# Kernel tuning notes

Measured on AMD Instinct MI355X. Metric: run time of the kernel, lower is better.

The kernel has to match this reference:

```python
import jax, jax.numpy as jnp
import numpy as np

D, B, N, DIM, H, DH, MLP = 6, 4, 1024, 768, 12, 64, 3072
SCALE = DH ** -0.5
EPS = 1e-5


def setup_inputs() -> dict:
    key = jax.random.key(0)
    ks = jax.random.split(key, 5)
    s = 0.02
    return {
        "x": jax.random.normal(ks[0], (B, N, DIM), jnp.float32),
        "ln1_g": jnp.ones((D, DIM), jnp.float32),
        "ln1_b": jnp.zeros((D, DIM), jnp.float32),
        "wqkv": jax.random.normal(ks[1], (D, DIM, 3 * H * DH), jnp.float32) * s,
        "wo": jax.random.normal(ks[2], (D, H * DH, DIM), jnp.float32) * s,
        "bo": jnp.zeros((D, DIM), jnp.float32),
        "ln2_g": jnp.ones((D, DIM), jnp.float32),
        "ln2_b": jnp.zeros((D, DIM), jnp.float32),
        "w1": jax.random.normal(ks[3], (D, DIM, MLP), jnp.float32) * s,
        "b1": jnp.zeros((D, MLP), jnp.float32),
        "w2": jax.random.normal(ks[4], (D, MLP, DIM), jnp.float32) * s,
        "b2": jnp.zeros((D, DIM), jnp.float32),
    }


def _ln(h, g, b):
    m = h.mean(-1, keepdims=True)
    v = h.var(-1, keepdims=True)  # biased, matches torch LayerNorm
    return (h - m) / jnp.sqrt(v + EPS) * g + b


def _heads(t):
    # [b, n, h*d] -> [b, h, n, d]
    return t.reshape(B, N, H, DH).transpose(0, 2, 1, 3)


def reference(x, ln1_g, ln1_b, wqkv, wo, bo, ln2_g, ln2_b, w1, b1, w2, b2):
    def step(carry, p):
        xc, _, _ = carry
        g1, be1, Wqkv, Wo, Bo, g2, be2, W1, B1, W2, B2 = p
        h = _ln(xc, g1, be1)
        q, k, v = jnp.split(h @ Wqkv, 3, axis=-1)
        q, k, v = _heads(q), _heads(k), _heads(v)
        attn = jax.nn.softmax(jnp.einsum('bhid,bhjd->bhij', q, k) * SCALE, axis=-1)
        out = jnp.einsum('bhij,bhjd->bhid', attn, v)
        out = out.transpose(0, 2, 1, 3).reshape(B, N, H * DH)
        xc = xc + out @ Wo + Bo
        h2 = _ln(xc, g2, be2)
        xc = xc + jax.nn.gelu(h2 @ W1 + B1, approximate=False) @ W2 + B2
        return (xc, k, v), None

    kv0 = jnp.zeros((B, H, N, DH), x.dtype)
    (xf, k, v), _ = jax.lax.scan(
        step, (x, kv0, kv0),
        (ln1_g, ln1_b, wqkv, wo, bo, ln2_g, ln2_b, w1, b1, w2, b2))
    return xf, k, v
```

## Files before the change

kernel.cpp:

```cpp
#include <hip/hip_runtime.h>
#include <hip/hip_bf16.h>
#include <math.h>

typedef __bf16 bf16;
typedef __bf16 bf16x8 __attribute__((ext_vector_type(8)));
typedef float f32x4 __attribute__((ext_vector_type(4)));

enum { EPI_QKV = 0, EPI_GELU = 1 };

__device__ __forceinline__ void gload16(const void* g, void* s) {
  __builtin_amdgcn_global_load_lds((__attribute__((address_space(1))) void*)g,
                                   (__attribute__((address_space(3))) void*)s, 16, 0, 0);
}

#define MFMA16(a, b, c) __builtin_amdgcn_mfma_f32_16x16x32_bf16((a), (b), (c), 0, 0, 0)

__device__ __forceinline__ void xcd_swizzle(int& bx, int& by) {
  const int gx = gridDim.x, nwg = gx * gridDim.y;
  int bid = blockIdx.y * gx + blockIdx.x;
  if ((nwg & 7) == 0) bid = (bid & 7) * (nwg >> 3) + (bid >> 3);
  bx = bid % gx;
  by = bid / gx;
}

__global__ __launch_bounds__(256) void cast_x(const float* __restrict__ x,
                                              float* __restrict__ xq) {
  const int i = (blockIdx.x * 256 + threadIdx.x) * 4;
  float4 v = *(const float4*)(x + i);
  v.x = (float)(bf16)v.x; v.y = (float)(bf16)v.y;
  v.z = (float)(bf16)v.z; v.w = (float)(bf16)v.w;
  *(float4*)(xq + i) = v;
}

__global__ __launch_bounds__(256) void wconv_all(
    const float* __restrict__ wqkv, const float* __restrict__ wo,
    const float* __restrict__ w1, const float* __restrict__ w2,
    bf16* __restrict__ qkvT, bf16* __restrict__ woT,
    bf16* __restrict__ w1T, bf16* __restrict__ w2T, int lfix) {
  __shared__ float tile[64][65];
  const int bid = blockIdx.x, t = threadIdx.x;
  int l, r;
  if (lfix < 0) { l = bid / 1728; r = bid % 1728; } else { l = lfix; r = bid; }
  const int lo = (lfix < 0) ? l : 0;
  const float* W; bf16* Wt; int K, N, tt;
  if (r < 432)       { W = wqkv + (size_t)l * 768 * 2304; Wt = qkvT + (size_t)lo * 2304 * 768; K = 768;  N = 2304; tt = r; }
  else if (r < 576)  { W = wo   + (size_t)l * 768 * 768;  Wt = woT  + (size_t)lo * 768 * 768;  K = 768;  N = 768;  tt = r - 432; }
  else if (r < 1152) { W = w1   + (size_t)l * 768 * 3072; Wt = w1T  + (size_t)lo * 3072 * 768; K = 768;  N = 3072; tt = r - 576; }
  else               { W = w2   + (size_t)l * 3072 * 768; Wt = w2T  + (size_t)lo * 768 * 3072; K = 3072; N = 768;  tt = r - 1152; }
  const int ntx = N >> 6;
  const int n0 = (tt % ntx) * 64, k0 = (tt / ntx) * 64;
  const int cx = (t & 15) * 4, ry = t >> 4;
#pragma unroll
  for (int pp = 0; pp < 4; ++pp) {
    const int row = ry + pp * 16;
    const float4 v = *(const float4*)(W + (size_t)(k0 + row) * N + n0 + cx);
    tile[row][cx] = v.x; tile[row][cx + 1] = v.y;
    tile[row][cx + 2] = v.z; tile[row][cx + 3] = v.w;
  }
  __syncthreads();
#pragma unroll
  for (int it = 0; it < 2; ++it) {
    const int c = it * 256 + t;
    const int n = c >> 3, kc = (c & 7) * 8;
    bf16x8 v;
#pragma unroll
    for (int j = 0; j < 8; ++j) v[j] = (bf16)tile[kc + j][n];
    *(bf16x8*)(Wt + (size_t)(n0 + n) * K + k0 + kc) = v;
  }
}

__global__ __launch_bounds__(256) void ln_kernel(const float* __restrict__ x,
                                                 const float* __restrict__ g,
                                                 const float* __restrict__ b,
                                                 bf16* __restrict__ out) {
  const int row = blockIdx.x, t = threadIdx.x;
  const float* xr = x + (size_t)row * 768;
  float v0 = xr[t], v1 = xr[t + 256], v2 = xr[t + 512];
  float s = v0 + v1 + v2, sq = v0 * v0 + v1 * v1 + v2 * v2;
#pragma unroll
  for (int m = 32; m; m >>= 1) { s += __shfl_xor(s, m); sq += __shfl_xor(sq, m); }
  __shared__ float rs[4], rq[4];
  const int w = t >> 6;
  if ((t & 63) == 0) { rs[w] = s; rq[w] = sq; }
  __syncthreads();
  s = rs[0] + rs[1] + rs[2] + rs[3];
  sq = rq[0] + rq[1] + rq[2] + rq[3];
  const float mean = s * (1.f / 768.f);
  const float var = sq * (1.f / 768.f) - mean * mean;
  const float rstd = rsqrtf(var + 1e-5f);
  bf16* orow = out + (size_t)row * 768;
  orow[t]       = (bf16)((v0 - mean) * rstd * g[t]       + b[t]);
  orow[t + 256] = (bf16)((v1 - mean) * rstd * g[t + 256] + b[t + 256]);
  orow[t + 512] = (bf16)((v2 - mean) * rstd * g[t + 512] + b[t + 512]);
}

template <int EPI>
__global__ __launch_bounds__(256) void gemm_s(
    const bf16* __restrict__ A, const bf16* __restrict__ Bt,
    const float* __restrict__ bias, bf16* __restrict__ Cb,
    bf16* __restrict__ qo, bf16* __restrict__ ko_, bf16* __restrict__ vo,
    float* __restrict__ kf, float* __restrict__ vf, int wf,
    int M, int Nc, int K) {
  __shared__ __align__(16) char lds[2][2][8192];
  const int t = threadIdx.x, lane = t & 63, w = t >> 6;
  const int wr = w >> 1, wc = w & 1;
  int bx, by;
  xcd_swizzle(bx, by);
  const size_t m0 = (size_t)by * 128, n0 = (size_t)bx * 128;

  const char* ab[2]; const char* bb[2];
#pragma unroll
  for (int r = 0; r < 2; ++r) {
    int c = r * 256 + t;
    ab[r] = (const char*)(A + (m0 + (c >> 2)) * (size_t)K) + (c & 3) * 16;
    bb[r] = (const char*)(Bt + (n0 + (c >> 2)) * (size_t)K) + (c & 3) * 16;
  }

  f32x4 acc[4][4] = {};

  auto stage = [&](int buf, int tt) {
#pragma unroll
    for (int r = 0; r < 2; ++r) {
      gload16(ab[r] + (size_t)tt * 64, &lds[buf][0][r * 4096 + w * 1024]);
      gload16(bb[r] + (size_t)tt * 64, &lds[buf][1][r * 4096 + w * 1024]);
    }
  };
  auto compute = [&](int buf) {
    const char* As = lds[buf][0];
    const char* Bs = lds[buf][1];
    const int ko = (lane >> 4) * 16;
    bf16x8 af[4], fb[4];
#pragma unroll
    for (int i = 0; i < 4; ++i) {
      af[i] = *(const bf16x8*)(As + (wr * 64 + i * 16 + (lane & 15)) * 64 + ko);
      fb[i] = *(const bf16x8*)(Bs + (wc * 64 + i * 16 + (lane & 15)) * 64 + ko);
    }
#pragma unroll
    for (int mi = 0; mi < 4; ++mi)
#pragma unroll
      for (int ni = 0; ni < 4; ++ni)
        acc[mi][ni] = MFMA16(af[mi], fb[ni], acc[mi][ni]);
  };

  const int NT = K >> 5;
  stage(0, 0);
  __syncthreads();
  int cur = 0;
  for (int tt = 1; tt < NT; ++tt) {
    stage(cur ^ 1, tt);
    compute(cur);
    __syncthreads();
    cur ^= 1;
  }
  compute(cur);

#pragma unroll
  for (int mi = 0; mi < 4; ++mi) {
#pragma unroll
    for (int i = 0; i < 4; ++i) {
      size_t row = m0 + wr * 64 + mi * 16 + ((lane >> 4) << 2) + i;
#pragma unroll
      for (int ni = 0; ni < 4; ++ni) {
        size_t col = n0 + wc * 64 + ni * 16 + (lane & 15);
        float v = acc[mi][ni][i];
        if (EPI == EPI_GELU) {
          v += bias[col];
          v = 0.5f * v * (1.f + erff(v * 0.70710678118f));
          Cb[row * (size_t)Nc + col] = (bf16)v;
        } else {
          int b = (int)(row >> 10), n = (int)(row & 1023);
          int which = (int)col >= 1536 ? 2 : ((int)col >= 768 ? 1 : 0);
          int hd = (int)col - which * 768;
          int hh = hd >> 6, d = hd & 63;
          size_t dst = ((size_t)(b * 12 + hh) * 1024 + n) * 64 + d;
          if (which == 0) {
            qo[dst] = (bf16)(v * 0.125f);
          } else if (which == 1) {
            ko_[dst] = (bf16)v;
            if (wf) kf[dst] = v;
          } else {
            vo[dst] = (bf16)v;
            if (wf) vf[dst] = v;
          }
        }
      }
    }
  }
}

__global__ __launch_bounds__(256) void gemm64_s(
    const bf16* __restrict__ A, const bf16* __restrict__ Bt,
    const float* __restrict__ bias, const float* __restrict__ res,
    float* __restrict__ Cf, int M, int Nc, int K) {
  __shared__ __align__(16) char lds[2][12288];
  const int t = threadIdx.x, lane = t & 63, w = t >> 6;
  const int wr = w >> 1, wc = w & 1;
  const int l15 = lane & 15, l4 = lane >> 4;
  int bx, by;
  xcd_swizzle(bx, by);
  const size_t m0 = (size_t)by * 64, n0 = (size_t)bx * 128;

  const char* ab = (const char*)(A + (m0 + (t >> 2)) * (size_t)K) + (t & 3) * 16;
  const char* b0 = (const char*)(Bt + (n0 + (t >> 2)) * (size_t)K) + (t & 3) * 16;
  const char* b1 = (const char*)(Bt + (n0 + 64 + (t >> 2)) * (size_t)K) + (t & 3) * 16;

  f32x4 acc[2][4] = {};

  auto stage = [&](int buf, int tt) {
    gload16(ab + (size_t)tt * 64, &lds[buf][t * 16]);
    gload16(b0 + (size_t)tt * 64, &lds[buf][4096 + t * 16]);
    gload16(b1 + (size_t)tt * 64, &lds[buf][8192 + t * 16]);
  };
  auto compute = [&](int buf) {
    const char* L = lds[buf];
    const int ko = l4 * 16;
    bf16x8 fa[2], fb[4];
#pragma unroll
    for (int mi = 0; mi < 2; ++mi)
      fa[mi] = *(const bf16x8*)(L + (wr * 32 + mi * 16 + l15) * 64 + ko);
#pragma unroll
    for (int ni = 0; ni < 4; ++ni)
      fb[ni] = *(const bf16x8*)(L + 4096 + (wc * 64 + ni * 16 + l15) * 64 + ko);
#pragma unroll
    for (int mi = 0; mi < 2; ++mi)
#pragma unroll
      for (int ni = 0; ni < 4; ++ni)
        acc[mi][ni] = MFMA16(fa[mi], fb[ni], acc[mi][ni]);
  };

  const int NT = K >> 5;
  stage(0, 0);
  __syncthreads();
  int cur = 0;
  for (int tt = 1; tt < NT; ++tt) {
    stage(cur ^ 1, tt);
    compute(cur);
    __syncthreads();
    cur ^= 1;
  }
  compute(cur);

#pragma unroll
  for (int mi = 0; mi < 2; ++mi) {
#pragma unroll
    for (int i = 0; i < 4; ++i) {
      size_t row = m0 + wr * 32 + mi * 16 + l4 * 4 + i;
#pragma unroll
      for (int ni = 0; ni < 4; ++ni) {
        size_t col = n0 + wc * 64 + ni * 16 + l15;
        float v = acc[mi][ni][i] + bias[col] + res[row * (size_t)Nc + col];
        Cf[row * (size_t)Nc + col] = v;
      }
    }
  }
}

__global__ __launch_bounds__(256) void vtrans(const bf16* __restrict__ v,
                                              bf16* __restrict__ vT) {
  __shared__ bf16 tile[32][33];
  const int tx = threadIdx.x, ty = threadIdx.y;
  const int bh = blockIdx.x, n0 = blockIdx.y * 32, d0 = blockIdx.z * 32;
  const bf16* vb = v + (size_t)bh * 1024 * 64;
  bf16* vTb = vT + (size_t)bh * 64 * 1024;
#pragma unroll
  for (int r = 0; r < 4; ++r)
    tile[ty + r * 8][tx] = vb[(size_t)(n0 + ty + r * 8) * 64 + d0 + tx];
  __syncthreads();
#pragma unroll
  for (int r = 0; r < 4; ++r)
    vTb[(size_t)(d0 + ty + r * 8) * 1024 + n0 + tx] = tile[tx][ty + r * 8];
}

__global__ __launch_bounds__(64) void attn_main(const bf16* __restrict__ q,
                                                const bf16* __restrict__ k,
                                                const bf16* __restrict__ vT,
                                                float* __restrict__ pO,
                                                float* __restrict__ pM,
                                                float* __restrict__ pL) {
  __shared__ __align__(16) char Ks[16384];
  __shared__ __align__(16) char Vs[16384];
  char* Ps = Ks;
  const int bh = blockIdx.x, qb = blockIdx.y, half = blockIdx.z;
  const int lane = threadIdx.x & 63;
  const int l15 = lane & 15, l4 = lane >> 4;

  const char* kp = (const char*)(k + (size_t)bh * 1024 * 64);
  const char* vp = (const char*)(vT + (size_t)bh * 64 * 1024);

  const char* kb0 = kp + (lane >> 3) * 128 + (((lane & 7) ^ ((lane >> 3) & 7)) * 16)
                  + (size_t)half * 4 * 16384;
  const int vr0 = lane >> 4;
  const char* vb0 = vp + (size_t)vr0 * 2048 + (((lane & 15) ^ vr0) * 16) + half * 4 * 256;
  const char* vb1 = vp + (size_t)(vr0 + 4) * 2048 + (((lane & 15) ^ (vr0 + 4)) * 16)
                  + half * 4 * 256;

  bf16x8 aq[2][2];
  {
    const bf16* qbase = q + ((size_t)bh * 1024 + qb * 32) * 64;
#pragma unroll
    for (int mi = 0; mi < 2; ++mi)
#pragma unroll
      for (int ks = 0; ks < 2; ++ks)
        aq[mi][ks] = *(const bf16x8*)(qbase + (mi * 16 + l15) * 64 + ks * 32 + l4 * 8);
  }

  bf16x8 vones;
#pragma unroll
  for (int j = 0; j < 8; ++j) vones[j] = (bf16)1.0f;

  f32x4 oacc[2][4] = {};
  f32x4 lacc[2] = {};
  float mrun[2][4];
#pragma unroll
  for (int mi = 0; mi < 2; ++mi)
#pragma unroll
    for (int i = 0; i < 4; ++i) mrun[mi][i] = -1e30f;

#pragma unroll
  for (int jb = 0; jb < 4; ++jb) {
    const char* ksrc = kb0 + (size_t)jb * 16384;
#pragma unroll
    for (int r = 0; r < 16; ++r)
      gload16(ksrc + r * 1024, &Ks[r * 1024]);
    const char* vsrc0 = vb0 + jb * 256;
    const char* vsrc1 = vb1 + jb * 256;
#pragma unroll
    for (int r = 0; r < 8; ++r) {
      gload16(vsrc0 + (size_t)r * 16384, &Vs[r * 2048]);
      gload16(vsrc1 + (size_t)r * 16384, &Vs[r * 2048 + 1024]);
    }
    asm volatile("s_waitcnt vmcnt(16)" ::: "memory");
    __builtin_amdgcn_sched_barrier(0);

    f32x4 sacc[2][8] = {};
#pragma unroll
    for (int ks = 0; ks < 2; ++ks) {
#pragma unroll
      for (int ni = 0; ni < 8; ++ni) {
        const int rr = ni * 16 + l15;
        const bf16x8 bk = *(const bf16x8*)(Ks + rr * 128 + (((ks * 4 + l4) ^ (rr & 7)) * 16));
        sacc[0][ni] = MFMA16(aq[0][ks], bk, sacc[0][ni]);
        sacc[1][ni] = MFMA16(aq[1][ks], bk, sacc[1][ni]);
      }
    }

#pragma unroll
    for (int mi = 0; mi < 2; ++mi) {
#pragma unroll
      for (int i = 0; i < 4; ++i) {
        float mx = sacc[mi][0][i];
#pragma unroll
        for (int ni = 1; ni < 8; ++ni) mx = fmaxf(mx, sacc[mi][ni][i]);
#pragma unroll
        for (int sh = 8; sh; sh >>= 1) mx = fmaxf(mx, __shfl_xor(mx, sh));
        float mnew = fmaxf(mrun[mi][i], mx);
        float alpha = __expf(mrun[mi][i] - mnew);
        mrun[mi][i] = mnew;
#pragma unroll
        for (int ni = 0; ni < 8; ++ni)
          sacc[mi][ni][i] = __expf(sacc[mi][ni][i] - mnew);
#pragma unroll
        for (int ni = 0; ni < 4; ++ni) oacc[mi][ni][i] *= alpha;
        lacc[mi][i] *= alpha;
      }
    }

#pragma unroll
    for (int mi = 0; mi < 2; ++mi)
#pragma unroll
      for (int i = 0; i < 4; ++i) {
        int rowl = mi * 16 + l4 * 4 + i;
        char* prp = Ps + rowl * 256;
        int sw = rowl & 7;
#pragma unroll
        for (int ni = 0; ni < 8; ++ni) {
          int col = ni * 16 + l15;
          *(bf16*)(prp + (((col >> 3) ^ sw) * 16) + (col & 7) * 2) = (bf16)sacc[mi][ni][i];
        }
      }

    asm volatile("s_waitcnt vmcnt(0)" ::: "memory");
    __builtin_amdgcn_sched_barrier(0);

    const int prow0 = l15, prow1 = 16 + l15;
#pragma unroll
    for (int ks = 0; ks < 4; ++ks) {
      const bf16x8 ap0 = *(const bf16x8*)(Ps + prow0 * 256 + (((ks * 4 + l4) ^ (prow0 & 7)) * 16));
      const bf16x8 ap1 = *(const bf16x8*)(Ps + prow1 * 256 + (((ks * 4 + l4) ^ (prow1 & 7)) * 16));
#pragma unroll
      for (int ni = 0; ni < 4; ++ni) {
        const int vr = ni * 16 + l15;
        const bf16x8 bv = *(const bf16x8*)(Vs + vr * 256 + (((ks * 4 + l4) ^ (vr & 7)) * 16));
        oacc[0][ni] = MFMA16(ap0, bv, oacc[0][ni]);
        oacc[1][ni] = MFMA16(ap1, bv, oacc[1][ni]);
      }
      lacc[0] = MFMA16(ap0, vones, lacc[0]);
      lacc[1] = MFMA16(ap1, vones, lacc[1]);
    }
  }

  const size_t pb = ((size_t)half * 1536 + bh * 32 + qb) * 32;
#pragma unroll
  for (int mi = 0; mi < 2; ++mi)
#pragma unroll
    for (int i = 0; i < 4; ++i) {
      const int row = mi * 16 + l4 * 4 + i;
      float* po = pO + (pb + row) * 64;
#pragma unroll
      for (int ni = 0; ni < 4; ++ni)
        po[ni * 16 + l15] = oacc[mi][ni][i];
      if (l15 == 0) {
        pM[pb + row] = mrun[mi][i];
        pL[pb + row] = lacc[mi][i];
      }
    }
}

__global__ __launch_bounds__(256) void attn_combine(const float* __restrict__ pO,
                                                    const float* __restrict__ pM,
                                                    const float* __restrict__ pL,
                                                    bf16* __restrict__ out) {
  const int blk = blockIdx.x;
  const int bh = blk >> 5, qb = blk & 31;
  const int t = threadIdx.x;
  const int row = t >> 3, d0 = (t & 7) * 8;
  const size_t base = (size_t)blk * 32 + row;
  const float m0 = pM[base], m1 = pM[49152 + base];
  const float M = fmaxf(m0, m1);
  const float s0 = __expf(m0 - M), s1 = __expf(m1 - M);
  const float L = pL[base] * s0 + pL[49152 + base] * s1;
  const float inv = 1.f / L;
  const float* p0 = pO + base * 64 + d0;
  const float* p1 = pO + (size_t)49152 * 64 + base * 64 + d0;
  const int b = bh / 12, hh = bh % 12;
  const int n = qb * 32 + row;
  bf16* orow = out + ((size_t)b * 1024 + n) * 768 + hh * 64 + d0;
  bf16x8 ov;
#pragma unroll
  for (int j = 0; j < 8; ++j)
    ov[j] = (bf16)((p0[j] * s0 + p1[j] * s1) * inv);
  *(bf16x8*)orow = ov;
}

extern "C" void kernel_launch(void* const* d_in, const int* in_sizes, int n_in,
                              void* d_out, int out_size, void* d_ws, size_t ws_size,
                              hipStream_t stream) {
  (void)in_sizes; (void)n_in; (void)out_size;
  const float* x_in = (const float*)d_in[0];
  const float* ln1g = (const float*)d_in[1];
  const float* ln1b = (const float*)d_in[2];
  const float* wqkv = (const float*)d_in[3];
  const float* wo   = (const float*)d_in[4];
  const float* bo   = (const float*)d_in[5];
  const float* ln2g = (const float*)d_in[6];
  const float* ln2b = (const float*)d_in[7];
  const float* w1   = (const float*)d_in[8];
  const float* b1   = (const float*)d_in[9];
  const float* w2   = (const float*)d_in[10];
  const float* b2   = (const float*)d_in[11];

  float* outx = (float*)d_out;
  float* outk = outx + (size_t)4096 * 768;
  float* outv = outk + (size_t)4096 * 768;

  char* p = (char*)d_ws;
  auto take = [&](size_t bytes) {
    char* r = p;
    p += (bytes + 255) & ~(size_t)255;
    return r;
  };
  float* xw   = (float*)take((size_t)4096 * 768 * 4);
  bf16*  h    = (bf16*)take((size_t)4096 * 768 * 2);
  bf16*  mbuf = (bf16*)take((size_t)4096 * 3072 * 2);
  bf16*  qbuf = (bf16*)take((size_t)4096 * 768 * 2);
  bf16*  kbuf = (bf16*)take((size_t)4096 * 768 * 2);
  bf16*  vbuf = (bf16*)take((size_t)4096 * 768 * 2);
  bf16*  vTb  = (bf16*)take((size_t)4096 * 768 * 2);
  bf16*  abuf = (bf16*)take((size_t)4096 * 768 * 2);
  float* pM   = (float*)take((size_t)2 * 49152 * 4);
  float* pL   = (float*)take((size_t)2 * 49152 * 4);
  float* pO   = (float*)mbuf;

  const size_t wq1 = (size_t)2304 * 768, wo1 = (size_t)768 * 768,
               w11 = (size_t)3072 * 768, w21 = (size_t)768 * 3072;
  const size_t used = (size_t)(p - (char*)d_ws);
  const size_t wbytes = (wq1 + wo1 + w11 + w21) * 2;
  const bool hoist = ws_size >= used + 6 * wbytes + 8192;
  const int nl = hoist ? 6 : 1;
  bf16* qkvT = (bf16*)take(wq1 * 2 * nl);
  bf16* woT  = (bf16*)take(wo1 * 2 * nl);
  bf16* w1T  = (bf16*)take(w11 * 2 * nl);
  bf16* w2T  = (bf16*)take(w21 * 2 * nl);

  cast_x<<<3072, 256, 0, stream>>>(x_in, xw);
  if (hoist)
    wconv_all<<<10368, 256, 0, stream>>>(wqkv, wo, w1, w2, qkvT, woT, w1T, w2T, -1);

  for (int l = 0; l < 6; ++l) {
    if (!hoist)
      wconv_all<<<1728, 256, 0, stream>>>(wqkv, wo, w1, w2, qkvT, woT, w1T, w2T, l);
    bf16* qkL = qkvT + (hoist ? (size_t)l * wq1 : 0);
    bf16* woL = woT  + (hoist ? (size_t)l * wo1 : 0);
    bf16* w1L = w1T  + (hoist ? (size_t)l * w11 : 0);
    bf16* w2L = w2T  + (hoist ? (size_t)l * w21 : 0);

    ln_kernel<<<4096, 256, 0, stream>>>(xw, ln1g + l * 768, ln1b + l * 768, h);
    gemm_s<EPI_QKV><<<dim3(18, 32), 256, 0, stream>>>(
        h, qkL, nullptr, nullptr, qbuf, kbuf, vbuf, outk, outv, l == 5 ? 1 : 0,
        4096, 2304, 768);
    vtrans<<<dim3(48, 32, 2), dim3(32, 8), 0, stream>>>(vbuf, vTb);
    attn_main<<<dim3(48, 32, 2), 64, 0, stream>>>(qbuf, kbuf, vTb, pO, pM, pL);
    attn_combine<<<1536, 256, 0, stream>>>(pO, pM, pL, abuf);
    gemm64_s<<<dim3(6, 64), 256, 0, stream>>>(
        abuf, woL, bo + l * 768, xw, xw, 4096, 768, 768);
    ln_kernel<<<4096, 256, 0, stream>>>(xw, ln2g + l * 768, ln2b + l * 768, h);
    gemm_s<EPI_GELU><<<dim3(24, 32), 256, 0, stream>>>(
        h, w1L, b1 + l * 3072, mbuf, nullptr, nullptr, nullptr, nullptr, nullptr, 0,
        4096, 3072, 768);
    gemm64_s<<<dim3(6, 64), 256, 0, stream>>>(
        mbuf, w2L, b2 + l * 768, xw, (l == 5) ? outx : xw, 4096, 768, 3072);
  }
}
```

Baseline: 1.235 ms.

## Split attention KV into four chunks and strip-mine weight conversion tiles

Attention now splits the key/value sequence four ways instead of two when the workspace can hold a dedicated partial-output buffer. This doubles the number of single-wave attention blocks to improve GPU occupancy, and the combine kernel now reduces over a variable number of partials. The weight conversion kernel processes four 64-column tiles per block with a double-buffered LDS tile and register prefetch, cutting its block count by four. The cost is more partial-result traffic and extra combine work per layer.

```diff
diff --git a/kernel.cpp b/kernel.cpp
--- a/kernel.cpp
+++ b/kernel.cpp
@@ -37,35 +37,47 @@
     const float* __restrict__ w1, const float* __restrict__ w2,
     bf16* __restrict__ qkvT, bf16* __restrict__ woT,
     bf16* __restrict__ w1T, bf16* __restrict__ w2T, int lfix) {
-  __shared__ float tile[64][65];
+  __shared__ float tile[2][64][65];
   const int bid = blockIdx.x, t = threadIdx.x;
   int l, r;
-  if (lfix < 0) { l = bid / 1728; r = bid % 1728; } else { l = lfix; r = bid; }
+  if (lfix < 0) { l = bid / 432; r = bid % 432; } else { l = lfix; r = bid; }
   const int lo = (lfix < 0) ? l : 0;
   const float* W; bf16* Wt; int K, N, tt;
-  if (r < 432)       { W = wqkv + (size_t)l * 768 * 2304; Wt = qkvT + (size_t)lo * 2304 * 768; K = 768;  N = 2304; tt = r; }
-  else if (r < 576)  { W = wo   + (size_t)l * 768 * 768;  Wt = woT  + (size_t)lo * 768 * 768;  K = 768;  N = 768;  tt = r - 432; }
-  else if (r < 1152) { W = w1   + (size_t)l * 768 * 3072; Wt = w1T  + (size_t)lo * 3072 * 768; K = 768;  N = 3072; tt = r - 576; }
-  else               { W = w2   + (size_t)l * 3072 * 768; Wt = w2T  + (size_t)lo * 768 * 3072; K = 3072; N = 768;  tt = r - 1152; }
-  const int ntx = N >> 6;
-  const int n0 = (tt % ntx) * 64, k0 = (tt / ntx) * 64;
+  if (r < 108)      { W = wqkv + (size_t)l * 768 * 2304; Wt = qkvT + (size_t)lo * 2304 * 768; K = 768;  N = 2304; tt = r; }
+  else if (r < 144) { W = wo   + (size_t)l * 768 * 768;  Wt = woT  + (size_t)lo * 768 * 768;  K = 768;  N = 768;  tt = r - 108; }
+  else if (r < 288) { W = w1   + (size_t)l * 768 * 3072; Wt = w1T  + (size_t)lo * 3072 * 768; K = 768;  N = 3072; tt = r - 144; }
+  else              { W = w2   + (size_t)l * 3072 * 768; Wt = w2T  + (size_t)lo * 768 * 3072; K = 3072; N = 768;  tt = r - 288; }
+  const int nstr = N >> 8;
+  const int n0 = (tt % nstr) * 256, k0 = (tt / nstr) * 64;
   const int cx = (t & 15) * 4, ry = t >> 4;
-#pragma unroll
-  for (int pp = 0; pp < 4; ++pp) {
-    const int row = ry + pp * 16;
-    const float4 v = *(const float4*)(W + (size_t)(k0 + row) * N + n0 + cx);
-    tile[row][cx] = v.x; tile[row][cx + 1] = v.y;
-    tile[row][cx + 2] = v.z; tile[row][cx + 3] = v.w;
-  }
-  __syncthreads();
-#pragma unroll
-  for (int it = 0; it < 2; ++it) {
-    const int c = it * 256 + t;
-    const int n = c >> 3, kc = (c & 7) * 8;
-    bf16x8 v;
-#pragma unroll
-    for (int j = 0; j < 8; ++j) v[j] = (bf16)tile[kc + j][n];
-    *(bf16x8*)(Wt + (size_t)(n0 + n) * K + k0 + kc) = v;
+
+  float4 v[4];
+  auto loadT = [&](int st) {
+#pragma unroll
+    for (int pp = 0; pp < 4; ++pp)
+      v[pp] = *(const float4*)(W + (size_t)(k0 + ry + pp * 16) * N + n0 + st * 64 + cx);
+  };
+  loadT(0);
+#pragma unroll
+  for (int st = 0; st < 4; ++st) {
+    float(*buf)[65] = tile[st & 1];
+#pragma unroll
+    for (int pp = 0; pp < 4; ++pp) {
+      const int row = ry + pp * 16;
+      buf[row][cx] = v[pp].x; buf[row][cx + 1] = v[pp].y;
+      buf[row][cx + 2] = v[pp].z; buf[row][cx + 3] = v[pp].w;
+    }
+    if (st < 3) loadT(st + 1);
+    __syncthreads();
+#pragma unroll
+    for (int it = 0; it < 2; ++it) {
+      const int c = it * 256 + t;
+      const int n = c >> 3, kc = (c & 7) * 8;
+      bf16x8 o;
+#pragma unroll
+      for (int j = 0; j < 8; ++j) o[j] = (bf16)buf[kc + j][n];
+      *(bf16x8*)(Wt + (size_t)(n0 + st * 64 + n) * K + k0 + kc) = o;
+    }
   }
 }
 
@@ -271,6 +283,7 @@
     vTb[(size_t)(d0 + ty + r * 8) * 1024 + n0 + tx] = tile[tx][ty + r * 8];
 }
 
+template <int KVB>
 __global__ __launch_bounds__(64) void attn_main(const bf16* __restrict__ q,
                                                 const bf16* __restrict__ k,
                                                 const bf16* __restrict__ vT,
@@ -280,7 +293,7 @@
   __shared__ __align__(16) char Ks[16384];
   __shared__ __align__(16) char Vs[16384];
   char* Ps = Ks;
-  const int bh = blockIdx.x, qb = blockIdx.y, half = blockIdx.z;
+  const int bh = blockIdx.x, qb = blockIdx.y, sp = blockIdx.z;
   const int lane = threadIdx.x & 63;
   const int l15 = lane & 15, l4 = lane >> 4;
 
@@ -288,11 +301,11 @@
   const char* vp = (const char*)(vT + (size_t)bh * 64 * 1024);
 
   const char* kb0 = kp + (lane >> 3) * 128 + (((lane & 7) ^ ((lane >> 3) & 7)) * 16)
-                  + (size_t)half * 4 * 16384;
+                  + (size_t)sp * KVB * 16384;
   const int vr0 = lane >> 4;
-  const char* vb0 = vp + (size_t)vr0 * 2048 + (((lane & 15) ^ vr0) * 16) + half * 4 * 256;
+  const char* vb0 = vp + (size_t)vr0 * 2048 + (((lane & 15) ^ vr0) * 16) + sp * KVB * 256;
   const char* vb1 = vp + (size_t)(vr0 + 4) * 2048 + (((lane & 15) ^ (vr0 + 4)) * 16)
-                  + half * 4 * 256;
+                  + sp * KVB * 256;
 
   bf16x8 aq[2][2];
   {
@@ -317,7 +330,7 @@
     for (int i = 0; i < 4; ++i) mrun[mi][i] = -1e30f;
 
 #pragma unroll
-  for (int jb = 0; jb < 4; ++jb) {
+  for (int jb = 0; jb < KVB; ++jb) {
     const char* ksrc = kb0 + (size_t)jb * 16384;
 #pragma unroll
     for (int r = 0; r < 16; ++r)
@@ -399,7 +412,7 @@
     }
   }
 
-  const size_t pb = ((size_t)half * 1536 + bh * 32 + qb) * 32;
+  const size_t pb = ((size_t)sp * 1536 + bh * 32 + qb) * 32;
 #pragma unroll
   for (int mi = 0; mi < 2; ++mi)
 #pragma unroll
@@ -419,26 +432,30 @@
 __global__ __launch_bounds__(256) void attn_combine(const float* __restrict__ pO,
                                                     const float* __restrict__ pM,
                                                     const float* __restrict__ pL,
-                                                    bf16* __restrict__ out) {
+                                                    bf16* __restrict__ out, int nspl) {
   const int blk = blockIdx.x;
   const int bh = blk >> 5, qb = blk & 31;
   const int t = threadIdx.x;
   const int row = t >> 3, d0 = (t & 7) * 8;
   const size_t base = (size_t)blk * 32 + row;
-  const float m0 = pM[base], m1 = pM[49152 + base];
-  const float M = fmaxf(m0, m1);
-  const float s0 = __expf(m0 - M), s1 = __expf(m1 - M);
-  const float L = pL[base] * s0 + pL[49152 + base] * s1;
+  float M = pM[base];
+  for (int p = 1; p < nspl; ++p) M = fmaxf(M, pM[(size_t)p * 49152 + base]);
+  float L = 0.f;
+  float o[8] = {};
+  for (int p = 0; p < nspl; ++p) {
+    const float sc = __expf(pM[(size_t)p * 49152 + base] - M);
+    L += pL[(size_t)p * 49152 + base] * sc;
+    const float* op = pO + ((size_t)p * 49152 + base) * 64 + d0;
+#pragma unroll
+    for (int j = 0; j < 8; ++j) o[j] += op[j] * sc;
+  }
   const float inv = 1.f / L;
-  const float* p0 = pO + base * 64 + d0;
-  const float* p1 = pO + (size_t)49152 * 64 + base * 64 + d0;
   const int b = bh / 12, hh = bh % 12;
   const int n = qb * 32 + row;
   bf16* orow = out + ((size_t)b * 1024 + n) * 768 + hh * 64 + d0;
   bf16x8 ov;
 #pragma unroll
-  for (int j = 0; j < 8; ++j)
-    ov[j] = (bf16)((p0[j] * s0 + p1[j] * s1) * inv);
+  for (int j = 0; j < 8; ++j) ov[j] = (bf16)(o[j] * inv);
   *(bf16x8*)orow = ov;
 }
 
@@ -477,28 +494,33 @@
   bf16*  vbuf = (bf16*)take((size_t)4096 * 768 * 2);
   bf16*  vTb  = (bf16*)take((size_t)4096 * 768 * 2);
   bf16*  abuf = (bf16*)take((size_t)4096 * 768 * 2);
-  float* pM   = (float*)take((size_t)2 * 49152 * 4);
-  float* pL   = (float*)take((size_t)2 * 49152 * 4);
-  float* pO   = (float*)mbuf;
+  float* pM   = (float*)take((size_t)4 * 49152 * 4);
+  float* pL   = (float*)take((size_t)4 * 49152 * 4);
 
   const size_t wq1 = (size_t)2304 * 768, wo1 = (size_t)768 * 768,
                w11 = (size_t)3072 * 768, w21 = (size_t)768 * 3072;
-  const size_t used = (size_t)(p - (char*)d_ws);
+  const size_t usedW = (size_t)(p - (char*)d_ws);
   const size_t wbytes = (wq1 + wo1 + w11 + w21) * 2;
-  const bool hoist = ws_size >= used + 6 * wbytes + 8192;
+  const bool hoist = ws_size >= usedW + 6 * wbytes + 8192;
   const int nl = hoist ? 6 : 1;
   bf16* qkvT = (bf16*)take(wq1 * 2 * nl);
   bf16* woT  = (bf16*)take(wo1 * 2 * nl);
   bf16* w1T  = (bf16*)take(w11 * 2 * nl);
   bf16* w2T  = (bf16*)take(w21 * 2 * nl);
 
+  const size_t po4 = (size_t)4 * 49152 * 64 * 4;
+  const size_t usedT = (size_t)(p - (char*)d_ws);
+  const bool split4 = ws_size >= usedT + po4 + 8192;
+  float* pO = split4 ? (float*)take(po4) : (float*)mbuf;
+  const int nspl = split4 ? 4 : 2;
+
   cast_x<<<3072, 256, 0, stream>>>(x_in, xw);
   if (hoist)
-    wconv_all<<<10368, 256, 0, stream>>>(wqkv, wo, w1, w2, qkvT, woT, w1T, w2T, -1);
+    wconv_all<<<2592, 256, 0, stream>>>(wqkv, wo, w1, w2, qkvT, woT, w1T, w2T, -1);
 
   for (int l = 0; l < 6; ++l) {
     if (!hoist)
-      wconv_all<<<1728, 256, 0, stream>>>(wqkv, wo, w1, w2, qkvT, woT, w1T, w2T, l);
+      wconv_all<<<432, 256, 0, stream>>>(wqkv, wo, w1, w2, qkvT, woT, w1T, w2T, l);
     bf16* qkL = qkvT + (hoist ? (size_t)l * wq1 : 0);
     bf16* woL = woT  + (hoist ? (size_t)l * wo1 : 0);
     bf16* w1L = w1T  + (hoist ? (size_t)l * w11 : 0);
@@ -509,8 +531,11 @@
         h, qkL, nullptr, nullptr, qbuf, kbuf, vbuf, outk, outv, l == 5 ? 1 : 0,
         4096, 2304, 768);
     vtrans<<<dim3(48, 32, 2), dim3(32, 8), 0, stream>>>(vbuf, vTb);
-    attn_main<<<dim3(48, 32, 2), 64, 0, stream>>>(qbuf, kbuf, vTb, pO, pM, pL);
-    attn_combine<<<1536, 256, 0, stream>>>(pO, pM, pL, abuf);
+    if (split4)
+      attn_main<2><<<dim3(48, 32, 4), 64, 0, stream>>>(qbuf, kbuf, vTb, pO, pM, pL);
+    else
+      attn_main<4><<<dim3(48, 32, 2), 64, 0, stream>>>(qbuf, kbuf, vTb, pO, pM, pL);
+    attn_combine<<<1536, 256, 0, stream>>>(pO, pM, pL, abuf, nspl);
     gemm64_s<<<dim3(6, 64), 256, 0, stream>>>(
         abuf, woL, bo + l * 768, xw, xw, 4096, 768, 768);
     ln_kernel<<<4096, 256, 0, stream>>>(xw, ln2g + l * 768, ln2b + l * 768, h);
```

After: 1.273 ms. 3.1% more time.
